# Kernel tuning notes

Measured on AMD Instinct MI355X. Metric: run time of the kernel, lower is better.

The kernel has to match this reference:

```python
import jax, jax.numpy as jnp
import numpy as np

N, E, F_IN, C, D = 50000, 200000, 384, 384, 16
NEG_SLOPE = 0.2


def setup_inputs() -> dict:
    key = jax.random.key(0)
    ks = jax.random.split(key, 12)
    x = jax.random.normal(ks[0], (N, F_IN), jnp.float32)
    # random edges with no self-loops (PyG GATConv removes self loops before re-adding them)
    src = jax.random.randint(ks[1], (E,), 0, N)
    off = jax.random.randint(ks[2], (E,), 1, N)
    dst = (src + off) % N
    edge_index = jnp.stack([src, dst]).astype(jnp.int32)  # [2, E]
    edge_attr = jax.random.uniform(ks[3], (E, D), jnp.float32)
    # GATConv params (heads=1): lin (no bias), att_src/att_dst/att_edge, lin_edge (no bias), bias
    W_lin = jax.random.normal(ks[4], (F_IN, C), jnp.float32) / np.float32(np.sqrt(F_IN))
    att_src = jax.random.normal(ks[5], (C,), jnp.float32) * 0.1
    att_dst = jax.random.normal(ks[6], (C,), jnp.float32) * 0.1
    W_edge = jax.random.normal(ks[7], (D, C), jnp.float32) / np.float32(np.sqrt(D))
    att_edge = jax.random.normal(ks[8], (C,), jnp.float32) * 0.1
    bias_conv = jnp.zeros((C,), jnp.float32)
    # final Linear(384 -> 1) with bias
    W_out = jax.random.normal(ks[9], (C, 1), jnp.float32) / np.float32(np.sqrt(C))
    b_out = jnp.zeros((1,), jnp.float32)
    return {"x": x, "edge_index": edge_index, "edge_attr": edge_attr,
            "W_lin": W_lin, "att_src": att_src, "att_dst": att_dst,
            "W_edge": W_edge, "att_edge": att_edge, "bias_conv": bias_conv,
            "W_out": W_out, "b_out": b_out}


def _gat_conv(x, edge_index, edge_attr, W_lin, att_src, att_dst, W_edge, att_edge, bias_conv):
    src, dst = edge_index[0], edge_index[1]
    h = x @ W_lin                              # [N, C]
    a_src = h @ att_src                        # [N]
    a_dst = h @ att_dst                        # [N]
    # add self loops; self-loop edge_attr = per-node mean of incoming edge_attr (fill_value='mean')
    deg = jax.ops.segment_sum(jnp.ones((E,), x.dtype), dst, num_segments=N)
    ea_mean = jax.ops.segment_sum(edge_attr, dst, num_segments=N) / jnp.maximum(deg, 1.0)[:, None]
    loop = jnp.arange(N, dtype=src.dtype)
    src_f = jnp.concatenate([src, loop])       # [E+N]
    dst_f = jnp.concatenate([dst, loop])
    ea_f = jnp.concatenate([edge_attr, ea_mean], axis=0)  # [E+N, D]
    a_edge = (ea_f @ W_edge) @ att_edge        # [E+N]
    # per-edge attention logits, segment softmax over destination neighborhoods
    alpha = jax.nn.leaky_relu(a_src[src_f] + a_dst[dst_f] + a_edge, NEG_SLOPE)
    amax = jax.ops.segment_max(alpha, dst_f, num_segments=N)  # every node has a self loop
    ex = jnp.exp(alpha - amax[dst_f])
    denom = jax.ops.segment_sum(ex, dst_f, num_segments=N)
    w = ex / denom[dst_f]                      # [E+N]
    # weighted scatter-aggregate of source messages
    out = jax.ops.segment_sum(h[src_f] * w[:, None], dst_f, num_segments=N)
    return out + bias_conv


def reference(x, edge_index, edge_attr, W_lin, att_src, att_dst, W_edge, att_edge, bias_conv, W_out, b_out):
    h = _gat_conv(x, edge_index, edge_attr, W_lin, att_src, att_dst, W_edge, att_edge, bias_conv)
    return jax.nn.relu(h @ W_out + b_out)      # [N, 1]
```

## Files before the change

### kernel.cpp

```cpp
#include <hip/hip_runtime.h>

#define NEG_SLOPE 0.2f
#define TPB    256
#define NB     256
#define CNT    196
#define EBLK   256
#define ER     4
#define MAGIC  21913099ULL
#define NBLK2  782
#define CHUNKCAP 1024
#define PSTRIDE  260

__device__ __forceinline__ float wsum64(float v) {
#pragma unroll
    for (int off = 1; off < 64; off <<= 1) v += __shfl_xor(v, off);
    return v;
}

__global__ __launch_bounds__(TPB) void k_fold(
        const float* __restrict__ Wlin, const float* __restrict__ att_src,
        const float* __restrict__ att_dst, const float* __restrict__ Wedge,
        const float* __restrict__ att_edge, const float* __restrict__ bias_conv,
        const float* __restrict__ Wout, const float* __restrict__ bout,
        float* __restrict__ vs, float* __restrict__ va, float* __restrict__ vb,
        float* __restrict__ we, float* __restrict__ cb) {
    const int gwid = (blockIdx.x * TPB + threadIdx.x) >> 6;
    const int lane = threadIdx.x & 63;
    if (gwid < 384) {
        int f = gwid;
        float a = 0.f, b = 0.f, c = 0.f;
        for (int k = lane; k < 384; k += 64) {
            float w = Wlin[f * 384 + k];
            a += w * Wout[k];
            b += w * att_src[k];
            c += w * att_dst[k];
        }
        a = wsum64(a); b = wsum64(b); c = wsum64(c);
        if (lane == 0) { vs[f] = a; va[f] = b; vb[f] = c; }
    } else if (gwid < 400) {
        int d = gwid - 384;
        float a = 0.f;
        for (int k = lane; k < 384; k += 64) a += Wedge[d * 384 + k] * att_edge[k];
        a = wsum64(a);
        if (lane == 0) we[d] = a;
    } else if (gwid == 400) {
        float a = 0.f;
        for (int k = lane; k < 384; k += 64) a += bias_conv[k] * Wout[k];
        a = wsum64(a);
        if (lane == 0) cb[0] = a + bout[0];
    }
}

__global__ __launch_bounds__(TPB) void k_node(
        const float* __restrict__ x,
        const float* __restrict__ vs, const float* __restrict__ va,
        const float* __restrict__ vb,
        float* __restrict__ s, float* __restrict__ asrc,
        float* __restrict__ adst, int N) {
    const int tid  = threadIdx.x;
    const int ll   = tid & 15;
    const int slot = blockIdx.x * 16 + (tid >> 4);
    const float4* vs4 = (const float4*)vs;
    const float4* va4 = (const float4*)va;
    const float4* vb4 = (const float4*)vb;
    float4 wsr[6], war[6], wbr[6];
#pragma unroll
    for (int j = 0; j < 6; ++j) {
        wsr[j] = vs4[ll + 16 * j];
        war[j] = va4[ll + 16 * j];
        wbr[j] = vb4[ll + 16 * j];
    }
#pragma unroll
    for (int i = 0; i < 4; ++i) {
        int n = slot + i * (NBLK2 * 16);
        if (n < N) {
            const float4* row = (const float4*)(x + (size_t)n * 384);
            float4 xr[6];
#pragma unroll
            for (int j = 0; j < 6; ++j) xr[j] = row[ll + 16 * j];
            float a = 0.f, b = 0.f, c = 0.f;
#pragma unroll
            for (int j = 0; j < 6; ++j) {
                a += xr[j].x*wsr[j].x + xr[j].y*wsr[j].y + xr[j].z*wsr[j].z + xr[j].w*wsr[j].w;
                b += xr[j].x*war[j].x + xr[j].y*war[j].y + xr[j].z*war[j].z + xr[j].w*war[j].w;
                c += xr[j].x*wbr[j].x + xr[j].y*wbr[j].y + xr[j].z*wbr[j].z + xr[j].w*wbr[j].w;
            }
#pragma unroll
            for (int off = 8; off > 0; off >>= 1) {
                a += __shfl_xor(a, off);
                b += __shfl_xor(b, off);
                c += __shfl_xor(c, off);
            }
            if (ll == 0) { s[n] = a; asrc[n] = b; adst[n] = c; }
        }
    }
}

__global__ __launch_bounds__(TPB) void k_edge(
        const int* __restrict__ src, const int* __restrict__ dst,
        const float* __restrict__ ea, const float* __restrict__ we,
        uint2* __restrict__ rec, int* __restrict__ cntP, int E) {
    __shared__ float weL[16];
    __shared__ int   ldsCnt[NB];
    __shared__ int   ldsOff[NB];
    __shared__ uint2 stage[CHUNKCAP];
    const int tid  = threadIdx.x;
    const int eblk = blockIdx.x;
    if (tid < 16) weL[tid] = we[tid];
    ldsCnt[tid] = 0;
    __syncthreads();

    const int chunk = (E + EBLK - 1) / EBLK;
    const int ebase = eblk * chunk;
    const int eend  = min(E, ebase + chunk);
    int dnr[ER], rkr[ER], bkr[ER];
#pragma unroll
    for (int r = 0; r < ER; ++r) {
        int e = ebase + r * TPB + tid;
        dnr[r] = -1;
        if (e < eend) {
            int dn = dnr[r] = dst[e];
            int b  = bkr[r] = (int)(((unsigned long long)(unsigned)dn * MAGIC) >> 32);
            rkr[r] = atomicAdd(&ldsCnt[b], 1);
        }
    }
    __syncthreads();
    const int creg = ldsCnt[tid];
#pragma unroll
    for (int d = 1; d < NB; d <<= 1) {
        int v = (tid >= d) ? ldsCnt[tid - d] : 0;
        __syncthreads();
        ldsCnt[tid] += v;
        __syncthreads();
    }
    ldsOff[tid] = ldsCnt[tid] - creg;
    __syncthreads();
    const int total = ldsCnt[NB - 1];

    const float4 w0 = make_float4(weL[0],  weL[1],  weL[2],  weL[3]);
    const float4 w1 = make_float4(weL[4],  weL[5],  weL[6],  weL[7]);
    const float4 w2 = make_float4(weL[8],  weL[9],  weL[10], weL[11]);
    const float4 w3 = make_float4(weL[12], weL[13], weL[14], weL[15]);
#pragma unroll
    for (int r = 0; r < ER; ++r) {
        int dn = dnr[r];
        if (dn >= 0) {
            int e  = ebase + r * TPB + tid;
            int sn = src[e];
            const float4* rw = (const float4*)(ea + (size_t)e * 16);
            float4 v0 = rw[0], v1 = rw[1], v2 = rw[2], v3 = rw[3];
            float a = v0.x*w0.x + v0.y*w0.y + v0.z*w0.z + v0.w*w0.w
                    + v1.x*w1.x + v1.y*w1.y + v1.z*w1.z + v1.w*w1.w
                    + v2.x*w2.x + v2.y*w2.y + v2.z*w2.z + v2.w*w2.w
                    + v3.x*w3.x + v3.y*w3.y + v3.z*w3.z + v3.w*w3.w;
            int b = bkr[r];
            unsigned key = ((unsigned)(dn - b * CNT) << 16) | (unsigned)sn;
            stage[ldsOff[b] + rkr[r]] = make_uint2(key, __float_as_uint(a));
        }
    }
    __syncthreads();
    uint2* dstc = rec + (size_t)eblk * CHUNKCAP;
    for (int i = tid; i < total; i += TPB) dstc[i] = stage[i];
    cntP[eblk * PSTRIDE + tid] = ldsOff[tid];
    if (tid == 0) cntP[eblk * PSTRIDE + NB] = total;
}

__global__ __launch_bounds__(TPB) void k_agg(
        const uint2* __restrict__ rec, const int* __restrict__ cntP,
        const float* __restrict__ asrc, const float* __restrict__ adst,
        const float* __restrict__ s, const float* __restrict__ cb,
        float* __restrict__ out, int n_nodes) {
    __shared__ float4 accL[CNT];
    __shared__ float  adstL[CNT];
    const int b  = blockIdx.x;
    const int lo = b * CNT;
    int cn = n_nodes - lo;
    if (cn <= 0) return;
    if (cn > CNT) cn = CNT;
    const int tid = threadIdx.x;
    for (int r = tid; r < CNT; r += TPB) accL[r] = make_float4(0.f, 0.f, 0.f, 0.f);
    for (int r = tid; r < cn; r += TPB)  adstL[r] = adst[lo + r];
    __syncthreads();
    const int p0 = cntP[tid * PSTRIDE + b];
    const int p1 = cntP[tid * PSTRIDE + b + 1];
    const uint2* base = rec + (size_t)tid * CHUNKCAP;
    for (int i = p0; i < p1; ++i) {
        uint2 rc = base[i];
        int r  = (int)(rc.x >> 16);
        int sn = (int)(rc.x & 0xFFFFu);
        float a  = __uint_as_float(rc.y);
        float al = asrc[sn] + adstL[r] + a;
        al = al >= 0.f ? al : NEG_SLOPE * al;
        float ex = __expf(al);
        float* bp = (float*)&accL[r];
        atomicAdd(bp + 0, 1.0f);
        atomicAdd(bp + 1, a);
        atomicAdd(bp + 2, ex);
        atomicAdd(bp + 3, ex * s[sn]);
    }
    __syncthreads();
    const float cbv = cb[0];
    for (int r = tid; r < cn; r += TPB) {
        int n = lo + r;
        float4 ac = accL[r];
        float d  = ac.x < 1.f ? 1.f : ac.x;
        float al = asrc[n] + adstL[r] + ac.y / d;
        al = al >= 0.f ? al : NEG_SLOPE * al;
        float ex = __expf(al);
        float v = (ac.w + ex * s[n]) / (ac.z + ex) + cbv;
        out[n] = v > 0.f ? v : 0.f;
    }
}

extern "C" void kernel_launch(void* const* d_in, const int* in_sizes, int n_in,
                              void* d_out, int out_size, void* d_ws, size_t ws_size,
                              hipStream_t stream) {
    const float* x        = (const float*)d_in[0];
    const int*   eidx     = (const int*)d_in[1];
    const float* ea       = (const float*)d_in[2];
    const float* Wlin     = (const float*)d_in[3];
    const float* att_src  = (const float*)d_in[4];
    const float* att_dst  = (const float*)d_in[5];
    const float* Wedge    = (const float*)d_in[6];
    const float* att_edge = (const float*)d_in[7];
    const float* bias_c   = (const float*)d_in[8];
    const float* Wout     = (const float*)d_in[9];
    const float* bout     = (const float*)d_in[10];
    float*       out      = (float*)d_out;

    const int N = in_sizes[0] / 384;
    const int E = in_sizes[2] / 16;
    const int* src = eidx;
    const int* dst = eidx + E;

    float* W = (float*)d_ws;
    float* vs   = W;
    float* va   = W + 384;
    float* vb   = W + 768;
    float* we   = W + 1152;
    float* cb   = W + 1168;
    float* s    = W + 1280;
    float* asrc = s + N;
    float* adst = asrc + N;
    int*   cntP = (int*)(adst + N);
    uint2* rec  = (uint2*)(cntP + EBLK * PSTRIDE);

    k_fold<<<101, TPB, 0, stream>>>(
        Wlin, att_src, att_dst, Wedge, att_edge, bias_c, Wout, bout,
        vs, va, vb, we, cb);
    k_node<<<NBLK2, TPB, 0, stream>>>(
        x, vs, va, vb, s, asrc, adst, N);
    k_edge<<<EBLK, TPB, 0, stream>>>(
        src, dst, ea, we, rec, cntP, E);
    k_agg<<<NB, TPB, 0, stream>>>(
        rec, cntP, asrc, adst, s, cb, out, N);
}
```

Before: 40.00 us.

## Widen edge and aggregation blocks to 1024 threads and double node-kernel grid

The node kernel now uses twice as many blocks, and each thread covers two nodes instead of four. The edge bucketing kernel runs 1024 threads per block, one edge per thread, in place of 256 threads each looping over four edges. The aggregation kernel also uses 1024 threads, with four threads striding through each producer chunk's records. The aim is more parallelism and latency hiding in these small-grid kernels. The costs are extra idle threads during the 256-wide scan and more LDS atomic contention on the accumulators.

```diff
diff --git a/kernel.cpp b/kernel.cpp
--- a/kernel.cpp
+++ b/kernel.cpp
@@ -2,12 +2,12 @@
 
 #define NEG_SLOPE 0.2f
 #define TPB    256
+#define TPB_E  1024
 #define NB     256
 #define CNT    196
 #define EBLK   256
-#define ER     4
 #define MAGIC  21913099ULL
-#define NBLK2  782
+#define NBLK3  1563
 #define CHUNKCAP 1024
 #define PSTRIDE  260
 
@@ -71,8 +71,8 @@
         wbr[j] = vb4[ll + 16 * j];
     }
 #pragma unroll
-    for (int i = 0; i < 4; ++i) {
-        int n = slot + i * (NBLK2 * 16);
+    for (int i = 0; i < 2; ++i) {
+        int n = slot + i * (NBLK3 * 16);
         if (n < N) {
             const float4* row = (const float4*)(x + (size_t)n * 384);
             float4 xr[6];
@@ -96,7 +96,7 @@
     }
 }
 
-__global__ __launch_bounds__(TPB) void k_edge(
+__global__ __launch_bounds__(TPB_E) void k_edge(
         const int* __restrict__ src, const int* __restrict__ dst,
         const float* __restrict__ ea, const float* __restrict__ we,
         uint2* __restrict__ rec, int* __restrict__ cntP, int E) {
@@ -107,65 +107,56 @@
     const int tid  = threadIdx.x;
     const int eblk = blockIdx.x;
     if (tid < 16) weL[tid] = we[tid];
-    ldsCnt[tid] = 0;
+    if (tid < NB) ldsCnt[tid] = 0;
     __syncthreads();
 
     const int chunk = (E + EBLK - 1) / EBLK;
     const int ebase = eblk * chunk;
     const int eend  = min(E, ebase + chunk);
-    int dnr[ER], rkr[ER], bkr[ER];
-#pragma unroll
-    for (int r = 0; r < ER; ++r) {
-        int e = ebase + r * TPB + tid;
-        dnr[r] = -1;
-        if (e < eend) {
-            int dn = dnr[r] = dst[e];
-            int b  = bkr[r] = (int)(((unsigned long long)(unsigned)dn * MAGIC) >> 32);
-            rkr[r] = atomicAdd(&ldsCnt[b], 1);
-        }
-    }
-    __syncthreads();
-    const int creg = ldsCnt[tid];
+    const int e     = ebase + tid;
+    const bool valid = e < eend;
+    int dn = 0, bk = 0, rk = 0;
+    if (valid) {
+        dn = dst[e];
+        bk = (int)(((unsigned long long)(unsigned)dn * MAGIC) >> 32);
+        rk = atomicAdd(&ldsCnt[bk], 1);
+    }
+    __syncthreads();
+    const int creg = (tid < NB) ? ldsCnt[tid] : 0;
 #pragma unroll
     for (int d = 1; d < NB; d <<= 1) {
-        int v = (tid >= d) ? ldsCnt[tid - d] : 0;
+        int v = (tid >= d && tid < NB) ? ldsCnt[tid - d] : 0;
         __syncthreads();
-        ldsCnt[tid] += v;
+        if (tid < NB) ldsCnt[tid] += v;
         __syncthreads();
     }
-    ldsOff[tid] = ldsCnt[tid] - creg;
+    if (tid < NB) ldsOff[tid] = ldsCnt[tid] - creg;
     __syncthreads();
     const int total = ldsCnt[NB - 1];
 
-    const float4 w0 = make_float4(weL[0],  weL[1],  weL[2],  weL[3]);
-    const float4 w1 = make_float4(weL[4],  weL[5],  weL[6],  weL[7]);
-    const float4 w2 = make_float4(weL[8],  weL[9],  weL[10], weL[11]);
-    const float4 w3 = make_float4(weL[12], weL[13], weL[14], weL[15]);
-#pragma unroll
-    for (int r = 0; r < ER; ++r) {
-        int dn = dnr[r];
-        if (dn >= 0) {
-            int e  = ebase + r * TPB + tid;
-            int sn = src[e];
-            const float4* rw = (const float4*)(ea + (size_t)e * 16);
-            float4 v0 = rw[0], v1 = rw[1], v2 = rw[2], v3 = rw[3];
-            float a = v0.x*w0.x + v0.y*w0.y + v0.z*w0.z + v0.w*w0.w
-                    + v1.x*w1.x + v1.y*w1.y + v1.z*w1.z + v1.w*w1.w
-                    + v2.x*w2.x + v2.y*w2.y + v2.z*w2.z + v2.w*w2.w
-                    + v3.x*w3.x + v3.y*w3.y + v3.z*w3.z + v3.w*w3.w;
-            int b = bkr[r];
-            unsigned key = ((unsigned)(dn - b * CNT) << 16) | (unsigned)sn;
-            stage[ldsOff[b] + rkr[r]] = make_uint2(key, __float_as_uint(a));
-        }
+    if (valid) {
+        const int sn = src[e];
+        const float4* rw = (const float4*)(ea + (size_t)e * 16);
+        const float4 w0 = make_float4(weL[0],  weL[1],  weL[2],  weL[3]);
+        const float4 w1 = make_float4(weL[4],  weL[5],  weL[6],  weL[7]);
+        const float4 w2 = make_float4(weL[8],  weL[9],  weL[10], weL[11]);
+        const float4 w3 = make_float4(weL[12], weL[13], weL[14], weL[15]);
+        float4 v0 = rw[0], v1 = rw[1], v2 = rw[2], v3 = rw[3];
+        float a = v0.x*w0.x + v0.y*w0.y + v0.z*w0.z + v0.w*w0.w
+                + v1.x*w1.x + v1.y*w1.y + v1.z*w1.z + v1.w*w1.w
+                + v2.x*w2.x + v2.y*w2.y + v2.z*w2.z + v2.w*w2.w
+                + v3.x*w3.x + v3.y*w3.y + v3.z*w3.z + v3.w*w3.w;
+        unsigned key = ((unsigned)(dn - bk * CNT) << 16) | (unsigned)sn;
+        stage[ldsOff[bk] + rk] = make_uint2(key, __float_as_uint(a));
     }
     __syncthreads();
     uint2* dstc = rec + (size_t)eblk * CHUNKCAP;
-    for (int i = tid; i < total; i += TPB) dstc[i] = stage[i];
-    cntP[eblk * PSTRIDE + tid] = ldsOff[tid];
+    if (tid < total) dstc[tid] = stage[tid];
+    if (tid < NB) cntP[eblk * PSTRIDE + tid] = ldsOff[tid];
     if (tid == 0) cntP[eblk * PSTRIDE + NB] = total;
 }
 
-__global__ __launch_bounds__(TPB) void k_agg(
+__global__ __launch_bounds__(TPB_E) void k_agg(
         const uint2* __restrict__ rec, const int* __restrict__ cntP,
         const float* __restrict__ asrc, const float* __restrict__ adst,
         const float* __restrict__ s, const float* __restrict__ cb,
@@ -178,13 +169,15 @@
     if (cn <= 0) return;
     if (cn > CNT) cn = CNT;
     const int tid = threadIdx.x;
-    for (int r = tid; r < CNT; r += TPB) accL[r] = make_float4(0.f, 0.f, 0.f, 0.f);
-    for (int r = tid; r < cn; r += TPB)  adstL[r] = adst[lo + r];
-    __syncthreads();
-    const int p0 = cntP[tid * PSTRIDE + b];
-    const int p1 = cntP[tid * PSTRIDE + b + 1];
-    const uint2* base = rec + (size_t)tid * CHUNKCAP;
-    for (int i = p0; i < p1; ++i) {
+    for (int r = tid; r < CNT; r += TPB_E) accL[r] = make_float4(0.f, 0.f, 0.f, 0.f);
+    for (int r = tid; r < cn; r += TPB_E)  adstL[r] = adst[lo + r];
+    __syncthreads();
+    const int eblk = tid & (NB - 1);
+    const int q    = tid >> 8;
+    const int p0 = cntP[eblk * PSTRIDE + b];
+    const int p1 = cntP[eblk * PSTRIDE + b + 1];
+    const uint2* base = rec + (size_t)eblk * CHUNKCAP;
+    for (int i = p0 + q; i < p1; i += 4) {
         uint2 rc = base[i];
         int r  = (int)(rc.x >> 16);
         int sn = (int)(rc.x & 0xFFFFu);
@@ -200,7 +193,7 @@
     }
     __syncthreads();
     const float cbv = cb[0];
-    for (int r = tid; r < cn; r += TPB) {
+    for (int r = tid; r < cn; r += TPB_E) {
         int n = lo + r;
         float4 ac = accL[r];
         float d  = ac.x < 1.f ? 1.f : ac.x;
@@ -248,10 +241,10 @@
     k_fold<<<101, TPB, 0, stream>>>(
         Wlin, att_src, att_dst, Wedge, att_edge, bias_c, Wout, bout,
         vs, va, vb, we, cb);
-    k_node<<<NBLK2, TPB, 0, stream>>>(
+    k_node<<<NBLK3, TPB, 0, stream>>>(
         x, vs, va, vb, s, asrc, adst, N);
-    k_edge<<<EBLK, TPB, 0, stream>>>(
+    k_edge<<<EBLK, TPB_E, 0, stream>>>(
         src, dst, ea, we, rec, cntP, E);
-    k_agg<<<NB, TPB, 0, stream>>>(
+    k_agg<<<NB, TPB_E, 0, stream>>>(
         rec, cntP, asrc, adst, s, cb, out, N);
 }
```

Result: faster. 37.73 us (-5.7%).
